# Kernel tuning notes

Hardware: AMD Instinct MI355X
Metric: run time of the kernel (lower is better)

## Reference

```python
import jax, jax.numpy as jnp
import numpy as np

N_NODES = 50000
N_EDGES = 800000
NUM_FEATS = 128
HIDDEN = 512
OUT = 2


def setup_inputs() -> dict:
    key = jax.random.key(0)
    k1, k2, k3, k4 = jax.random.split(key, 4)
    X = jax.random.normal(k1, (N_NODES, NUM_FEATS), dtype=jnp.float32)
    edge_index = jax.random.randint(k2, (2, N_EDGES), 0, N_NODES, dtype=jnp.int64)
    W1 = jax.random.normal(k3, (NUM_FEATS, HIDDEN), dtype=jnp.float32) / np.sqrt(NUM_FEATS)
    b1 = jnp.zeros((HIDDEN,), dtype=jnp.float32)
    W2 = jax.random.normal(k4, (HIDDEN, OUT), dtype=jnp.float32) / np.sqrt(HIDDEN)
    b2 = jnp.zeros((OUT,), dtype=jnp.float32)
    return {"X": X, "edge_index": edge_index, "W1": W1, "b1": b1, "W2": W2, "b2": b2}


def _gcn_conv(x, W, b, src, dst, dinv, n):
    # PyG GCNConv: x' = D^{-1/2} (A + I) D^{-1/2} (x W) + b
    xw = x @ W  # [N, C]
    edge_norm = dinv[src] * dinv[dst]  # [E]
    msg = xw[src] * edge_norm[:, None]  # [E, C] gathered messages
    agg = jax.ops.segment_sum(msg, dst, num_segments=n)
    agg = agg + xw * (dinv * dinv)[:, None]  # self-loop contribution
    return agg + b


def reference(X, edge_index, W1, b1, W2, b2):
    n = X.shape[0]
    src, dst = edge_index[0], edge_index[1]
    # degree with self-loops (gcn_norm): deg[i] = in_degree(i) + 1
    deg = jax.ops.segment_sum(jnp.ones_like(dst, dtype=X.dtype), dst, num_segments=n) + 1.0
    dinv = jax.lax.rsqrt(deg)
    h = jax.nn.relu(_gcn_conv(X, W1, b1, src, dst, dinv, n))
    logits = _gcn_conv(h, W2, b2, src, dst, dinv, n)
    # nn.Softmax() on a 2D tensor defaults to dim=1
    return jax.nn.softmax(logits, axis=1)
```

## Files before the change

kernel.cpp:

```cpp
#include <hip/hip_runtime.h>

#define N_FEATS 128
#define HIDDEN 512
#define NPAD 50176
#define ELLW 64
#define NBKT 196
#define SLAB 4608

typedef __attribute__((ext_vector_type(4))) float floatx4;
typedef __attribute__((ext_vector_type(8))) short shortx8;

__device__ __forceinline__ unsigned short f2bf(float f) {
    union { float f; unsigned u; } a; a.f = f;
    unsigned r = a.u + 0x7fff + ((a.u >> 16) & 1);
    return (unsigned short)(r >> 16);
}

#define XH_BLOCKS 6250
__global__ __launch_bounds__(256) void k_init(const float* __restrict__ W1,
        unsigned short* __restrict__ w1t, const float* __restrict__ X,
        unsigned short* __restrict__ Xh, int* __restrict__ bcur, int N) {
    int b = blockIdx.x, tid = threadIdx.x;
    if (b < 16) {
        __shared__ unsigned short t[64][65];
        int ki = b >> 3, ni = b & 7;
        #pragma unroll
        for (int i = 0; i < 16; ++i) {
            int idx = tid + i * 256;
            int r = idx >> 6, c = idx & 63;
            t[r][c] = f2bf(W1[(ki * 64 + r) * 512 + ni * 64 + c]);
        }
        __syncthreads();
        #pragma unroll
        for (int i = 0; i < 16; ++i) {
            int idx = tid + i * 256;
            int rn = idx >> 6, ck = idx & 63;
            w1t[(ni * 64 + rn) * 128 + ki * 64 + ck] = t[ck][rn];
        }
    } else if (b == 16) {
        if (tid < 256) bcur[tid] = 0;
    } else {
        int idx = (b - 17) * 256 + tid;
        if (idx < N * 32) {
            float4 v = reinterpret_cast<const float4*>(X)[idx];
            ushort4 o;
            o.x = f2bf(v.x); o.y = f2bf(v.y); o.z = f2bf(v.z); o.w = f2bf(v.w);
            reinterpret_cast<ushort4*>(Xh)[idx] = o;
        }
    }
}

#define PA_EPB 4096
__global__ __launch_bounds__(256) void k_bucketA(const int* __restrict__ src,
        const int* __restrict__ dst, int* __restrict__ bcur,
        unsigned* __restrict__ staging, int E) {
    __shared__ int hist[NBKT];
    __shared__ int base[NBKT];
    int tid = threadIdx.x;
    int e0 = blockIdx.x * PA_EPB;
    for (int i = tid; i < NBKT; i += 256) hist[i] = 0;
    __syncthreads();
    #pragma unroll
    for (int i = 0; i < 16; ++i) {
        int e = e0 + tid + i * 256;
        if (e < E) atomicAdd(&hist[dst[e] >> 8], 1);
    }
    __syncthreads();
    for (int i = tid; i < NBKT; i += 256) {
        int c = hist[i];
        base[i] = c ? atomicAdd(&bcur[i], c) : 0;
        hist[i] = 0;
    }
    __syncthreads();
    #pragma unroll
    for (int i = 0; i < 16; ++i) {
        int e = e0 + tid + i * 256;
        if (e < E) {
            int d = dst[e];
            int bk = d >> 8;
            int r = atomicAdd(&hist[bk], 1);
            int pos = base[bk] + r;
            if (pos < SLAB)
                staging[(size_t)bk * SLAB + pos] = ((unsigned)src[e] << 8) | (unsigned)(d & 255);
        }
    }
}

__global__ __launch_bounds__(256) void k_bucketB(const int* __restrict__ bcur,
        const unsigned* __restrict__ staging, int* __restrict__ ell,
        int* __restrict__ cursor) {
    __shared__ int cur[256];
    int b = blockIdx.x, tid = threadIdx.x;
    cur[tid] = 0;
    __syncthreads();
    int cnt = bcur[b];
    if (cnt > SLAB) cnt = SLAB;
    for (int j = tid; j < cnt; j += 256) {
        unsigned v = staging[(size_t)b * SLAB + j];
        int dl = (int)(v & 255u);
        int s = (int)(v >> 8);
        int pos = atomicAdd(&cur[dl], 1);
        if (pos < ELLW) ell[(size_t)((b << 8) + dl) * ELLW + pos] = s;
    }
    __syncthreads();
    cursor[(b << 8) + tid] = cur[tid];
}

__global__ __launch_bounds__(256) void k_gather(const int* __restrict__ cursor,
        const int* __restrict__ ell, const unsigned short* __restrict__ Xh,
        unsigned short* __restrict__ aggAh, int N) {
    int t = blockIdx.x * 256 + threadIdx.x;
    int node = t >> 5;
    int lane = t & 31;
    if (node >= N) return;
    int cnt = cursor[node];
    float dv = rsqrtf((float)cnt + 1.0f);
    int lim = cnt < ELLW ? cnt : ELLW;
    const ushort4* Xv = reinterpret_cast<const ushort4*>(Xh);
    union { ushort4 u; unsigned short s[4]; } sv;
    sv.u = Xv[(size_t)node * 32 + lane];
    float a0, a1, a2, a3;
    {
        union { unsigned u; float f; } c0, c1, c2, c3;
        c0.u = (unsigned)sv.s[0] << 16; c1.u = (unsigned)sv.s[1] << 16;
        c2.u = (unsigned)sv.s[2] << 16; c3.u = (unsigned)sv.s[3] << 16;
        a0 = dv * c0.f; a1 = dv * c1.f; a2 = dv * c2.f; a3 = dv * c3.f;
    }
    const int* row = ell + (size_t)node * ELLW;
    int j = 0;
    #define BF(x) ({ union { unsigned u; float f; } _c; _c.u = (unsigned)(x) << 16; _c.f; })
    for (; j + 4 <= lim; j += 4) {
        int4 s4 = *reinterpret_cast<const int4*>(row + j);
        float w0 = rsqrtf((float)cursor[s4.x] + 1.0f);
        float w1 = rsqrtf((float)cursor[s4.y] + 1.0f);
        float w2 = rsqrtf((float)cursor[s4.z] + 1.0f);
        float w3 = rsqrtf((float)cursor[s4.w] + 1.0f);
        union { ushort4 u; unsigned short s[4]; } u0, u1, u2, u3;
        u0.u = Xv[(size_t)s4.x * 32 + lane];
        u1.u = Xv[(size_t)s4.y * 32 + lane];
        u2.u = Xv[(size_t)s4.z * 32 + lane];
        u3.u = Xv[(size_t)s4.w * 32 + lane];
        a0 += w0 * BF(u0.s[0]) + w1 * BF(u1.s[0]) + w2 * BF(u2.s[0]) + w3 * BF(u3.s[0]);
        a1 += w0 * BF(u0.s[1]) + w1 * BF(u1.s[1]) + w2 * BF(u2.s[1]) + w3 * BF(u3.s[1]);
        a2 += w0 * BF(u0.s[2]) + w1 * BF(u1.s[2]) + w2 * BF(u2.s[2]) + w3 * BF(u3.s[2]);
        a3 += w0 * BF(u0.s[3]) + w1 * BF(u1.s[3]) + w2 * BF(u2.s[3]) + w3 * BF(u3.s[3]);
    }
    for (; j < lim; ++j) {
        int s = row[j];
        float w = rsqrtf((float)cursor[s] + 1.0f);
        union { ushort4 u; unsigned short s4[4]; } u;
        u.u = Xv[(size_t)s * 32 + lane];
        a0 += w * BF(u.s4[0]); a1 += w * BF(u.s4[1]);
        a2 += w * BF(u.s4[2]); a3 += w * BF(u.s4[3]);
    }
    #undef BF
    ushort4 o;
    o.x = f2bf(a0 * dv); o.y = f2bf(a1 * dv); o.z = f2bf(a2 * dv); o.w = f2bf(a3 * dv);
    reinterpret_cast<ushort4*>(aggAh)[(size_t)node * 32 + lane] = o;
}

__global__ __launch_bounds__(256) void k_fused_mfma(
        const unsigned short* __restrict__ aggAh, const unsigned short* __restrict__ w1t,
        const float* __restrict__ b1, const float* __restrict__ W2,
        float* __restrict__ lp, int N) {
    __shared__ unsigned short As[64][136];
    __shared__ unsigned short Bs[128][136];
    __shared__ float b1s[HIDDEN];
    __shared__ float W2s[HIDDEN * 2];

    const int tid = threadIdx.x;
    const int wave = tid >> 6;
    const int lane = tid & 63;
    const int quad = lane >> 4;
    const int l16 = lane & 15;
    const int m0 = blockIdx.x * 64;

    for (int i = tid; i < HIDDEN; i += 256) b1s[i] = b1[i];
    for (int i = tid; i < HIDDEN * 2; i += 256) W2s[i] = W2[i];

    #pragma unroll
    for (int it = 0; it < 4; ++it) {
        int flat = (tid + it * 256) * 8;
        int r = flat >> 7, c = flat & 127;
        int gm = m0 + r;
        shortx8 v = {0, 0, 0, 0, 0, 0, 0, 0};
        if (gm < N) v = *reinterpret_cast<const shortx8*>(aggAh + (size_t)gm * 128 + c);
        *reinterpret_cast<shortx8*>(&As[r][c]) = v;
    }

    float accL0[4], accL1[4];
    #pragma unroll
    for (int r = 0; r < 4; ++r) { accL0[r] = 0.f; accL1[r] = 0.f; }

    for (int n0 = 0; n0 < HIDDEN; n0 += 128) {
        #pragma unroll
        for (int it = 0; it < 8; ++it) {
            int flat = (tid + it * 256) * 8;
            int r = flat >> 7, c = flat & 127;
            *reinterpret_cast<shortx8*>(&Bs[r][c]) =
                *reinterpret_cast<const shortx8*>(w1t + (size_t)(n0 + r) * 128 + c);
        }
        __syncthreads();

        floatx4 acc[8];
        #pragma unroll
        for (int nt = 0; nt < 8; ++nt) acc[nt] = (floatx4){0.f, 0.f, 0.f, 0.f};

        #pragma unroll
        for (int ks = 0; ks < 4; ++ks) {
            shortx8 af = *reinterpret_cast<const shortx8*>(&As[wave * 16 + l16][ks * 32 + quad * 8]);
            #pragma unroll
            for (int nt = 0; nt < 8; ++nt) {
                shortx8 bf = *reinterpret_cast<const shortx8*>(&Bs[nt * 16 + l16][ks * 32 + quad * 8]);
                acc[nt] = __builtin_amdgcn_mfma_f32_16x16x32_bf16(af, bf, acc[nt], 0, 0, 0);
            }
        }

        #pragma unroll
        for (int nt = 0; nt < 8; ++nt) {
            int col = n0 + nt * 16 + l16;
            float bb = b1s[col];
            float w20 = W2s[col * 2 + 0];
            float w21 = W2s[col * 2 + 1];
            #pragma unroll
            for (int r = 0; r < 4; ++r) {
                float h = acc[nt][r] + bb;
                h = h > 0.f ? h : 0.f;
                accL0[r] += h * w20;
                accL1[r] += h * w21;
            }
        }
        __syncthreads();
    }

    #pragma unroll
    for (int off = 1; off < 16; off <<= 1) {
        #pragma unroll
        for (int r = 0; r < 4; ++r) {
            accL0[r] += __shfl_xor(accL0[r], off);
            accL1[r] += __shfl_xor(accL1[r], off);
        }
    }
    if (l16 == 0) {
        #pragma unroll
        for (int r = 0; r < 4; ++r) {
            int gm = m0 + wave * 16 + quad * 4 + r;
            if (gm < N) {
                lp[(size_t)gm * 2 + 0] = accL0[r];
                lp[(size_t)gm * 2 + 1] = accL1[r];
            }
        }
    }
}

__global__ __launch_bounds__(256) void k_final(const int* __restrict__ cursor,
        const int* __restrict__ ell, const float* __restrict__ lp,
        const float* __restrict__ b2, float* __restrict__ out, int N) {
    int t = blockIdx.x * 256 + threadIdx.x;
    int node = t >> 3;
    int lane = t & 7;
    if (node >= N) return;
    int cnt = cursor[node];
    int lim = cnt < ELLW ? cnt : ELLW;
    const int* row = ell + (size_t)node * ELLW;
    float a0 = 0.f, a1 = 0.f;
    for (int j = lane; j < lim; j += 8) {
        int s = row[j];
        float w = rsqrtf((float)cursor[s] + 1.0f);
        a0 += w * lp[(size_t)s * 2 + 0];
        a1 += w * lp[(size_t)s * 2 + 1];
    }
    #pragma unroll
    for (int off = 1; off < 8; off <<= 1) {
        a0 += __shfl_xor(a0, off);
        a1 += __shfl_xor(a1, off);
    }
    if (lane == 0) {
        float dv = rsqrtf((float)cnt + 1.0f);
        float l0 = dv * (a0 + dv * lp[(size_t)node * 2 + 0]) + b2[0];
        float l1 = dv * (a1 + dv * lp[(size_t)node * 2 + 1]) + b2[1];
        float m = fmaxf(l0, l1);
        float e0 = __expf(l0 - m), e1 = __expf(l1 - m);
        float inv = 1.0f / (e0 + e1);
        out[(size_t)node * 2 + 0] = e0 * inv;
        out[(size_t)node * 2 + 1] = e1 * inv;
    }
}

extern "C" void kernel_launch(void* const* d_in, const int* in_sizes, int n_in,
                              void* d_out, int out_size, void* d_ws, size_t ws_size,
                              hipStream_t stream) {
    const float* X  = (const float*)d_in[0];
    const int* ei   = (const int*)d_in[1];
    const float* W1 = (const float*)d_in[2];
    const float* b1 = (const float*)d_in[3];
    const float* W2 = (const float*)d_in[4];
    const float* b2 = (const float*)d_in[5];
    float* out = (float*)d_out;

    const int N = in_sizes[0] / N_FEATS;
    const int E = in_sizes[1] / 2;
    const int* src = ei;
    const int* dst = ei + E;

    int* cursor = (int*)d_ws;
    int* bcur   = cursor + NPAD;
    int* ell    = bcur + 256;
    float* lp   = (float*)(ell + (size_t)NPAD * ELLW);
    unsigned short* w1t = (unsigned short*)(lp + 2 * NPAD);
    unsigned short* Xh  = w1t + 512 * 128;
    unsigned* staging = (unsigned*)(Xh + (size_t)NPAD * 128);
    unsigned short* aggAh = (unsigned short*)staging;

    k_init    <<<17 + XH_BLOCKS, 256, 0, stream>>>(W1, w1t, X, Xh, bcur, N);
    k_bucketA <<<(E + PA_EPB - 1) / PA_EPB, 256, 0, stream>>>(src, dst, bcur, staging, E);
    k_bucketB <<<NBKT, 256, 0, stream>>>(bcur, staging, ell, cursor);
    k_gather  <<<((size_t)N * 32 + 255) / 256, 256, 0, stream>>>(cursor, ell, Xh, aggAh, N);
    k_fused_mfma<<<(N + 63) / 64, 256, 0, stream>>>(aggAh, w1t, b1, W2, lp, N);
    k_final   <<<((size_t)N * 8 + 255) / 256, 256, 0, stream>>>(cursor, ell, lp, b2, out, N);
}
```

Before: 175.8 us.

## Precompute dinv per node, vectorize bucket loads, double MFMA row tile

Computes 1/sqrt(deg+1) once per node in the bucketing kernel and stores it, so gather and final kernels read a float instead of running rsqrt on cursor values per edge. The bucket histogram and scatter passes now load dst/src as int4 vectors. The fused MFMA kernel doubles its row tile to 128 so each wave handles two 16-row A fragments and reuses each B fragment twice. This raises accumulator register and LDS use and halves the block count, which could lower occupancy.

Result: faster. 169.3 us (-3.7%).

```diff
diff --git a/kernel.cpp b/kernel.cpp
--- a/kernel.cpp
+++ b/kernel.cpp
@@ -57,13 +57,21 @@
     __shared__ int hist[NBKT];
     __shared__ int base[NBKT];
     int tid = threadIdx.x;
-    int e0 = blockIdx.x * PA_EPB;
     for (int i = tid; i < NBKT; i += 256) hist[i] = 0;
     __syncthreads();
     #pragma unroll
-    for (int i = 0; i < 16; ++i) {
-        int e = e0 + tid + i * 256;
-        if (e < E) atomicAdd(&hist[dst[e] >> 8], 1);
+    for (int i = 0; i < 4; ++i) {
+        int e = blockIdx.x * PA_EPB + (i * 256 + tid) * 4;
+        if (e + 3 < E) {
+            int4 d4 = *reinterpret_cast<const int4*>(dst + e);
+            atomicAdd(&hist[d4.x >> 8], 1);
+            atomicAdd(&hist[d4.y >> 8], 1);
+            atomicAdd(&hist[d4.z >> 8], 1);
+            atomicAdd(&hist[d4.w >> 8], 1);
+        } else {
+            for (int k = 0; k < 4; ++k)
+                if (e + k < E) atomicAdd(&hist[dst[e + k] >> 8], 1);
+        }
     }
     __syncthreads();
     for (int i = tid; i < NBKT; i += 256) {
@@ -73,22 +81,26 @@
     }
     __syncthreads();
     #pragma unroll
-    for (int i = 0; i < 16; ++i) {
-        int e = e0 + tid + i * 256;
-        if (e < E) {
-            int d = dst[e];
-            int bk = d >> 8;
-            int r = atomicAdd(&hist[bk], 1);
-            int pos = base[bk] + r;
-            if (pos < SLAB)
-                staging[(size_t)bk * SLAB + pos] = ((unsigned)src[e] << 8) | (unsigned)(d & 255);
+    for (int i = 0; i < 4; ++i) {
+        int e = blockIdx.x * PA_EPB + (i * 256 + tid) * 4;
+        if (e + 3 < E) {
+            int4 d4 = *reinterpret_cast<const int4*>(dst + e);
+            int4 s4 = *reinterpret_cast<const int4*>(src + e);
+            #define PUT(dd, ss) { int bk = (dd) >> 8; int r = atomicAdd(&hist[bk], 1); \
+                int pos = base[bk] + r; if (pos < SLAB) \
+                staging[(size_t)bk * SLAB + pos] = ((unsigned)(ss) << 8) | (unsigned)((dd) & 255); }
+            PUT(d4.x, s4.x) PUT(d4.y, s4.y) PUT(d4.z, s4.z) PUT(d4.w, s4.w)
+        } else {
+            for (int k = 0; k < 4; ++k)
+                if (e + k < E) { int dd = dst[e + k], ss = src[e + k]; PUT(dd, ss) }
+            #undef PUT
         }
     }
 }
 
 __global__ __launch_bounds__(256) void k_bucketB(const int* __restrict__ bcur,
         const unsigned* __restrict__ staging, int* __restrict__ ell,
-        int* __restrict__ cursor) {
+        int* __restrict__ cursor, float* __restrict__ dinvs) {
     __shared__ int cur[256];
     int b = blockIdx.x, tid = threadIdx.x;
     cur[tid] = 0;
@@ -103,38 +115,32 @@
         if (pos < ELLW) ell[(size_t)((b << 8) + dl) * ELLW + pos] = s;
     }
     __syncthreads();
-    cursor[(b << 8) + tid] = cur[tid];
+    int c = cur[tid];
+    cursor[(b << 8) + tid] = c;
+    dinvs[(b << 8) + tid] = rsqrtf((float)c + 1.0f);
 }
 
 __global__ __launch_bounds__(256) void k_gather(const int* __restrict__ cursor,
-        const int* __restrict__ ell, const unsigned short* __restrict__ Xh,
-        unsigned short* __restrict__ aggAh, int N) {
+        const float* __restrict__ dinvs, const int* __restrict__ ell,
+        const unsigned short* __restrict__ Xh, unsigned short* __restrict__ aggAh, int N) {
     int t = blockIdx.x * 256 + threadIdx.x;
     int node = t >> 5;
     int lane = t & 31;
     if (node >= N) return;
     int cnt = cursor[node];
-    float dv = rsqrtf((float)cnt + 1.0f);
+    float dv = dinvs[node];
     int lim = cnt < ELLW ? cnt : ELLW;
     const ushort4* Xv = reinterpret_cast<const ushort4*>(Xh);
+    #define BF(x) ({ union { unsigned u; float f; } _c; _c.u = (unsigned)(x) << 16; _c.f; })
     union { ushort4 u; unsigned short s[4]; } sv;
     sv.u = Xv[(size_t)node * 32 + lane];
-    float a0, a1, a2, a3;
-    {
-        union { unsigned u; float f; } c0, c1, c2, c3;
-        c0.u = (unsigned)sv.s[0] << 16; c1.u = (unsigned)sv.s[1] << 16;
-        c2.u = (unsigned)sv.s[2] << 16; c3.u = (unsigned)sv.s[3] << 16;
-        a0 = dv * c0.f; a1 = dv * c1.f; a2 = dv * c2.f; a3 = dv * c3.f;
-    }
+    float a0 = dv * BF(sv.s[0]), a1 = dv * BF(sv.s[1]);
+    float a2 = dv * BF(sv.s[2]), a3 = dv * BF(sv.s[3]);
     const int* row = ell + (size_t)node * ELLW;
     int j = 0;
-    #define BF(x) ({ union { unsigned u; float f; } _c; _c.u = (unsigned)(x) << 16; _c.f; })
     for (; j + 4 <= lim; j += 4) {
         int4 s4 = *reinterpret_cast<const int4*>(row + j);
-        float w0 = rsqrtf((float)cursor[s4.x] + 1.0f);
-        float w1 = rsqrtf((float)cursor[s4.y] + 1.0f);
-        float w2 = rsqrtf((float)cursor[s4.z] + 1.0f);
-        float w3 = rsqrtf((float)cursor[s4.w] + 1.0f);
+        float w0 = dinvs[s4.x], w1 = dinvs[s4.y], w2 = dinvs[s4.z], w3 = dinvs[s4.w];
         union { ushort4 u; unsigned short s[4]; } u0, u1, u2, u3;
         u0.u = Xv[(size_t)s4.x * 32 + lane];
         u1.u = Xv[(size_t)s4.y * 32 + lane];
@@ -147,7 +153,7 @@
     }
     for (; j < lim; ++j) {
         int s = row[j];
-        float w = rsqrtf((float)cursor[s] + 1.0f);
+        float w = dinvs[s];
         union { ushort4 u; unsigned short s4[4]; } u;
         u.u = Xv[(size_t)s * 32 + lane];
         a0 += w * BF(u.s4[0]); a1 += w * BF(u.s4[1]);
@@ -163,7 +169,7 @@
         const unsigned short* __restrict__ aggAh, const unsigned short* __restrict__ w1t,
         const float* __restrict__ b1, const float* __restrict__ W2,
         float* __restrict__ lp, int N) {
-    __shared__ unsigned short As[64][136];
+    __shared__ unsigned short As[128][136];
     __shared__ unsigned short Bs[128][136];
     __shared__ float b1s[HIDDEN];
     __shared__ float W2s[HIDDEN * 2];
@@ -173,13 +179,13 @@
     const int lane = tid & 63;
     const int quad = lane >> 4;
     const int l16 = lane & 15;
-    const int m0 = blockIdx.x * 64;
+    const int m0 = blockIdx.x * 128;
 
     for (int i = tid; i < HIDDEN; i += 256) b1s[i] = b1[i];
     for (int i = tid; i < HIDDEN * 2; i += 256) W2s[i] = W2[i];
 
     #pragma unroll
-    for (int it = 0; it < 4; ++it) {
+    for (int it = 0; it < 8; ++it) {
         int flat = (tid + it * 256) * 8;
         int r = flat >> 7, c = flat & 127;
         int gm = m0 + r;
@@ -188,9 +194,11 @@
         *reinterpret_cast<shortx8*>(&As[r][c]) = v;
     }
 
-    float accL0[4], accL1[4];
-    #pragma unroll
-    for (int r = 0; r < 4; ++r) { accL0[r] = 0.f; accL1[r] = 0.f; }
+    float accL0[2][4], accL1[2][4];
+    #pragma unroll
+    for (int s = 0; s < 2; ++s)
+        #pragma unroll
+        for (int r = 0; r < 4; ++r) { accL0[s][r] = 0.f; accL1[s][r] = 0.f; }
 
     for (int n0 = 0; n0 < HIDDEN; n0 += 128) {
         #pragma unroll
@@ -202,17 +210,21 @@
         }
         __syncthreads();
 
-        floatx4 acc[8];
-        #pragma unroll
-        for (int nt = 0; nt < 8; ++nt) acc[nt] = (floatx4){0.f, 0.f, 0.f, 0.f};
+        floatx4 acc[2][8];
+        #pragma unroll
+        for (int s = 0; s < 2; ++s)
+            #pragma unroll
+            for (int nt = 0; nt < 8; ++nt) acc[s][nt] = (floatx4){0.f, 0.f, 0.f, 0.f};
 
         #pragma unroll
         for (int ks = 0; ks < 4; ++ks) {
-            shortx8 af = *reinterpret_cast<const shortx8*>(&As[wave * 16 + l16][ks * 32 + quad * 8]);
+            shortx8 af0 = *reinterpret_cast<const shortx8*>(&As[wave * 32 + l16][ks * 32 + quad * 8]);
+            shortx8 af1 = *reinterpret_cast<const shortx8*>(&As[wave * 32 + 16 + l16][ks * 32 + quad * 8]);
             #pragma unroll
             for (int nt = 0; nt < 8; ++nt) {
                 shortx8 bf = *reinterpret_cast<const shortx8*>(&Bs[nt * 16 + l16][ks * 32 + quad * 8]);
-                acc[nt] = __builtin_amdgcn_mfma_f32_16x16x32_bf16(af, bf, acc[nt], 0, 0, 0);
+                acc[0][nt] = __builtin_amdgcn_mfma_f32_16x16x32_bf16(af0, bf, acc[0][nt], 0, 0, 0);
+                acc[1][nt] = __builtin_amdgcn_mfma_f32_16x16x32_bf16(af1, bf, acc[1][nt], 0, 0, 0);
             }
         }
 
@@ -223,39 +235,47 @@
             float w20 = W2s[col * 2 + 0];
             float w21 = W2s[col * 2 + 1];
             #pragma unroll
+            for (int s = 0; s < 2; ++s) {
+                #pragma unroll
+                for (int r = 0; r < 4; ++r) {
+                    float h = acc[s][nt][r] + bb;
+                    h = h > 0.f ? h : 0.f;
+                    accL0[s][r] += h * w20;
+                    accL1[s][r] += h * w21;
+                }
+            }
+        }
+        __syncthreads();
+    }
+
+    #pragma unroll
+    for (int off = 1; off < 16; off <<= 1) {
+        #pragma unroll
+        for (int s = 0; s < 2; ++s)
+            #pragma unroll
             for (int r = 0; r < 4; ++r) {
-                float h = acc[nt][r] + bb;
-                h = h > 0.f ? h : 0.f;
-                accL0[r] += h * w20;
-                accL1[r] += h * w21;
+                accL0[s][r] += __shfl_xor(accL0[s][r], off);
+                accL1[s][r] += __shfl_xor(accL1[s][r], off);
             }
-        }
-        __syncthreads();
-    }
-
-    #pragma unroll
-    for (int off = 1; off < 16; off <<= 1) {
-        #pragma unroll
-        for (int r = 0; r < 4; ++r) {
-            accL0[r] += __shfl_xor(accL0[r], off);
-            accL1[r] += __shfl_xor(accL1[r], off);
-        }
     }
     if (l16 == 0) {
         #pragma unroll
-        for (int r = 0; r < 4; ++r) {
-            int gm = m0 + wave * 16 + quad * 4 + r;
-            if (gm < N) {
-                lp[(size_t)gm * 2 + 0] = accL0[r];
-                lp[(size_t)gm * 2 + 1] = accL1[r];
+        for (int s = 0; s < 2; ++s)
+            #pragma unroll
+            for (int r = 0; r < 4; ++r) {
+                int gm = m0 + wave * 32 + s * 16 + quad * 4 + r;
+                if (gm < N) {
+                    lp[(size_t)gm * 2 + 0] = accL0[s][r];
+                    lp[(size_t)gm * 2 + 1] = accL1[s][r];
+                }
             }
-        }
     }
 }
 
 __global__ __launch_bounds__(256) void k_final(const int* __restrict__ cursor,
-        const int* __restrict__ ell, const float* __restrict__ lp,
-        const float* __restrict__ b2, float* __restrict__ out, int N) {
+        const float* __restrict__ dinvs, const int* __restrict__ ell,
+        const float* __restrict__ lp, const float* __restrict__ b2,
+        float* __restrict__ out, int N) {
     int t = blockIdx.x * 256 + threadIdx.x;
     int node = t >> 3;
     int lane = t & 7;
@@ -266,7 +286,7 @@
     float a0 = 0.f, a1 = 0.f;
     for (int j = lane; j < lim; j += 8) {
         int s = row[j];
-        float w = rsqrtf((float)cursor[s] + 1.0f);
+        float w = dinvs[s];
         a0 += w * lp[(size_t)s * 2 + 0];
         a1 += w * lp[(size_t)s * 2 + 1];
     }
@@ -276,7 +296,7 @@
         a1 += __shfl_xor(a1, off);
     }
     if (lane == 0) {
-        float dv = rsqrtf((float)cnt + 1.0f);
+        float dv = dinvs[node];
         float l0 = dv * (a0 + dv * lp[(size_t)node * 2 + 0]) + b2[0];
         float l1 = dv * (a1 + dv * lp[(size_t)node * 2 + 1]) + b2[1];
         float m = fmaxf(l0, l1);
@@ -307,15 +327,16 @@
     int* bcur   = cursor + NPAD;
     int* ell    = bcur + 256;
     float* lp   = (float*)(ell + (size_t)NPAD * ELLW);
-    unsigned short* w1t = (unsigned short*)(lp + 2 * NPAD);
+    float* dinvs = lp + 2 * NPAD;
+    unsigned short* w1t = (unsigned short*)(dinvs + NPAD);
     unsigned short* Xh  = w1t + 512 * 128;
     unsigned* staging = (unsigned*)(Xh + (size_t)NPAD * 128);
     unsigned short* aggAh = (unsigned short*)staging;
 
     k_init    <<<17 + XH_BLOCKS, 256, 0, stream>>>(W1, w1t, X, Xh, bcur, N);
     k_bucketA <<<(E + PA_EPB - 1) / PA_EPB, 256, 0, stream>>>(src, dst, bcur, staging, E);
-    k_bucketB <<<NBKT, 256, 0, stream>>>(bcur, staging, ell, cursor);
-    k_gather  <<<((size_t)N * 32 + 255) / 256, 256, 0, stream>>>(cursor, ell, Xh, aggAh, N);
-    k_fused_mfma<<<(N + 63) / 64, 256, 0, stream>>>(aggAh, w1t, b1, W2, lp, N);
-    k_final   <<<((size_t)N * 8 + 255) / 256, 256, 0, stream>>>(cursor, ell, lp, b2, out, N);
-}
+    k_bucketB <<<NBKT, 256, 0, stream>>>(bcur, staging, ell, cursor, dinvs);
+    k_gather  <<<((size_t)N * 32 + 255) / 256, 256, 0, stream>>>(cursor, dinvs, ell, Xh, aggAh, N);
+    k_fused_mfma<<<(N + 127) / 128, 256, 0, stream>>>(aggAh, w1t, b1, W2, lp, N);
+    k_final   <<<((size_t)N * 8 + 255) / 256, 256, 0, stream>>>(cursor, dinvs, ell, lp, b2, out, N);
+}
```
